# Kernel optimization log

Hardware: AMD Instinct MI355X
Metric: run time of the kernel (lower is better)

The kernel has to match this reference:

```python
import jax, jax.numpy as jnp
import numpy as np

B, T, C, H = 4, 4096, 1024, 128

def setup_inputs() -> dict:
    key = jax.random.key(0)
    k1, k2, k3, k4 = jax.random.split(key, 4)
    x = jax.random.normal(k1, (B, T, C), dtype=jnp.float32)
    # nn.Linear(embed, head, bias=False): y = x @ W, store W as [C, H]
    s = 1.0 / np.sqrt(C)
    Wk = jax.random.normal(k2, (C, H), dtype=jnp.float32) * s
    Wq = jax.random.normal(k3, (C, H), dtype=jnp.float32) * s
    Wv = jax.random.normal(k4, (C, H), dtype=jnp.float32) * s
    return {"x": x, "Wk": Wk, "Wq": Wq, "Wv": Wv}

def reference(x, Wk, Wq, Wv):
    Bx, Tx, Cx = x.shape
    scale = Wk.shape[1] ** -0.5
    k = x @ Wk  # [B,T,H]
    q = x @ Wq
    v = x @ Wv
    att = jnp.einsum('bth,bsh->bts', q, k) * scale  # [B,T,T]
    causal = jnp.triu(jnp.ones((Tx, Tx), dtype=bool), k=1)
    att = jnp.where(causal, -jnp.inf, att)
    att = jax.nn.softmax(att, axis=-1)
    # dropout is identity in eval mode
    out = jnp.einsum('bts,bsh->bth', att, v)  # [B,T,H]
    return out
```

## Files before the change

### kernel.cpp

```cpp
#include <hip/hip_runtime.h>
#include <stdint.h>
#include <math.h>

#define B_ 4
#define T_ 4096
#define C_ 1024
#define H_ 128

typedef __attribute__((ext_vector_type(8))) short s16x8;
typedef __attribute__((ext_vector_type(4))) float f32x4;

__device__ __forceinline__ unsigned short f2bf(float f) {
    union { float f; unsigned u; } v; v.f = f;
    unsigned r = v.u + 0x7fffu + ((v.u >> 16) & 1u);
    return (unsigned short)(r >> 16);
}

__device__ __forceinline__ s16x8 as_frag(uint4 u) {
    union { uint4 u; s16x8 s; } v; v.u = u; return v.s;
}

__host__ __device__ constexpr int chunks_total(int CH) {
    int a = 64 / CH, b = 64 % CH;
    return CH * a * (a + 1) / 2 + b * (a + 1);
}

#define QSC (0.0883883476f * 1.4426950408f)

__global__ __launch_bounds__(256) void k_wt(const float* __restrict__ Wk,
                                            const float* __restrict__ Wq,
                                            const float* __restrict__ Wv,
                                            unsigned short* __restrict__ Wt) {
    __shared__ float tile[64][65];
    int w = blockIdx.z;
    const float* W = (w == 0) ? Wk : (w == 1) ? Wq : Wv;
    int c0 = blockIdx.x * 64, h0 = blockIdx.y * 64;
    int tid = threadIdx.x;
#pragma unroll
    for (int k = 0; k < 16; k++) {
        int idx = tid + k * 256;
        int r = idx >> 6, c = idx & 63;
        tile[r][c] = W[(size_t)(c0 + r) * H_ + h0 + c];
    }
    __syncthreads();
#pragma unroll
    for (int k = 0; k < 16; k++) {
        int idx = tid + k * 256;
        int hh = idx >> 6, cc = idx & 63;
        Wt[(size_t)(w * H_ + h0 + hh) * C_ + c0 + cc] = f2bf(tile[cc][hh]);
    }
}

__global__ __launch_bounds__(512, 4) void k_qkv(const float* __restrict__ x,
                                                const unsigned short* __restrict__ Wt,
                                                unsigned short* __restrict__ Qb,
                                                unsigned short* __restrict__ Kb,
                                                unsigned short* __restrict__ Vt) {
    __shared__ unsigned short a_lds[2][32 * 72];
    int tid = threadIdx.x;
    int wv = tid >> 6, lane = tid & 63, quad = lane >> 4, lo = lane & 15;
    int r0 = blockIdx.x * 32;

    f32x4 acc[3][2];
#pragma unroll
    for (int i = 0; i < 3; i++)
#pragma unroll
        for (int j = 0; j < 2; j++) acc[i][j] = (f32x4){0.f, 0.f, 0.f, 0.f};

    const int row_s = tid >> 4;
    const int seg_s = (tid & 15) * 4;
    size_t xbase = (size_t)(r0 + row_s) * C_ + seg_s;

    const unsigned short* wp[3];
#pragma unroll
    for (int nt = 0; nt < 3; nt++)
        wp[nt] = Wt + (size_t)((wv * 3 + nt) * 16 + lo) * C_ + quad * 8;

    auto load_x = [&](int kc) -> float4 {
        return *(const float4*)(x + xbase + kc * 64);
    };
    auto pack_store = [&](unsigned short* buf, float4 f) {
        uint2 u;
        u.x = (unsigned)f2bf(f.x) | ((unsigned)f2bf(f.y) << 16);
        u.y = (unsigned)f2bf(f.z) | ((unsigned)f2bf(f.w) << 16);
        *(uint2*)&buf[row_s * 72 + seg_s] = u;
    };
    auto compute = [&](const unsigned short* buf, int kc) {
        s16x8 b[3][2];
#pragma unroll
        for (int nt = 0; nt < 3; nt++)
#pragma unroll
            for (int kh = 0; kh < 2; kh++)
                b[nt][kh] = *(const s16x8*)(wp[nt] + kc * 64 + kh * 32);
        s16x8 af[2][2];
#pragma unroll
        for (int mt = 0; mt < 2; mt++)
#pragma unroll
            for (int kh = 0; kh < 2; kh++)
                af[mt][kh] = *(const s16x8*)&buf[(mt * 16 + lo) * 72 + kh * 32 + quad * 8];
#pragma unroll
        for (int nt = 0; nt < 3; nt++)
#pragma unroll
            for (int kh = 0; kh < 2; kh++)
#pragma unroll
                for (int mt = 0; mt < 2; mt++)
                    acc[nt][mt] = __builtin_amdgcn_mfma_f32_16x16x32_bf16(
                        af[mt][kh], b[nt][kh], acc[nt][mt], 0, 0, 0);
    };

    float4 p0 = load_x(0);
    float4 p1 = load_x(1);
    pack_store(a_lds[0], p0);
    __syncthreads();

    for (int kc2 = 0; kc2 < 8; kc2++) {
        int kc = kc2 * 2;
        if (kc + 2 < 16) p0 = load_x(kc + 2);
        compute(a_lds[0], kc);
        pack_store(a_lds[1], p1);
        __syncthreads();
        if (kc + 3 < 16) p1 = load_x(kc + 3);
        compute(a_lds[1], kc + 1);
        if (kc + 2 < 16) pack_store(a_lds[0], p0);
        __syncthreads();
    }

#pragma unroll
    for (int nt = 0; nt < 3; nt++) {
        int col = (wv * 3 + nt) * 16 + lo;
        int w = col >> 7, h = col & 127;
#pragma unroll
        for (int mt = 0; mt < 2; mt++) {
            int mrow = r0 + mt * 16 + quad * 4;
            if (w == 2) {
                int b = mrow >> 12, t0 = mrow & 4095;
                int tp = (t0 & ~31) + (((t0 & 15) >> 2) << 3) + (((t0 >> 4) & 1) << 2);
                uint2 pk;
                pk.x = (unsigned)f2bf(acc[nt][mt][0]) | ((unsigned)f2bf(acc[nt][mt][1]) << 16);
                pk.y = (unsigned)f2bf(acc[nt][mt][2]) | ((unsigned)f2bf(acc[nt][mt][3]) << 16);
                *(uint2*)(Vt + (size_t)(b * H_ + h) * T_ + tp) = pk;
            } else if (w == 1) {
                unsigned short* dst = Qb + (size_t)mrow * H_ + h;
#pragma unroll
                for (int r = 0; r < 4; r++)
                    dst[(size_t)r * H_] = f2bf(acc[nt][mt][r] * QSC);
            } else {
                unsigned short* dst = Kb + (size_t)mrow * H_ + h;
#pragma unroll
                for (int r = 0; r < 4; r++)
                    dst[(size_t)r * H_] = f2bf(acc[nt][mt][r]);
            }
        }
    }
}

#define LOAD_KV(kv0)                                                            \
    do {                                                                        \
        const uint4* kg = (const uint4*)(Kb + (size_t)(batch * T_ + (kv0) + srow_k) * H_); \
        pk0 = kg[sseg_k + 0]; pk1 = kg[sseg_k + 1];                             \
        pk2 = kg[sseg_k + 2]; pk3 = kg[sseg_k + 3];                             \
        const uint4* vg = (const uint4*)(Vt + (size_t)(batch * H_ + srow_v) * T_ + (kv0)); \
        pv0 = vg[sseg_v + 0]; pv1 = vg[sseg_v + 1];                             \
        pv2 = vg[sseg_v + 2]; pv3 = vg[sseg_v + 3];                             \
    } while (0)

template <int CH>
__global__ __launch_bounds__(256, 3) void k_attn(const unsigned short* __restrict__ Qb,
                                                 const unsigned short* __restrict__ Kb,
                                                 const unsigned short* __restrict__ Vt,
                                                 float* __restrict__ Opart,
                                                 float* __restrict__ Mpart,
                                                 float* __restrict__ Lpart,
                                                 float* __restrict__ out) {
    __shared__ uint4 kbuf[64 * 16];
    __shared__ uint4 vbuf[128 * 8];

    int tid = threadIdx.x;
    int wv = tid >> 6, lane = tid & 63, quad = lane >> 4, lo = lane & 15;

    int id = blockIdx.x;
    int qt, batch, tbeg, tend, slot = 0;
    if constexpr (CH > 0) {
        slot = id >> 2; batch = id & 3;
        int s = slot, q = 63;
        for (;;) { int nc = (q + CH) / CH; if (s < nc) break; s -= nc; --q; }
        qt = q;
        tbeg = s * CH;
        tend = min(tbeg + CH, qt + 1);
    } else {
        qt = 63 - (id >> 2); batch = id & 3;
        tbeg = 0; tend = qt + 1;
    }
    int m0 = qt * 64 + wv * 16;
    int query = m0 + lo;

    s16x8 qf[4];
    size_t qrow = (size_t)(batch * T_ + m0 + lo) * H_;
#pragma unroll
    for (int ks = 0; ks < 4; ks++)
        qf[ks] = *(const s16x8*)(Qb + qrow + ks * 32 + quad * 8);

    f32x4 acc_o[8];
#pragma unroll
    for (int o = 0; o < 8; o++) acc_o[o] = (f32x4){0.f, 0.f, 0.f, 0.f};
    float m_i = -INFINITY, l_i = 0.f;

    const int srow_k = tid >> 2, sseg_k = (tid & 3) * 4;
    const int srow_v = tid >> 1, sseg_v = (tid & 1) * 4;

    uint4 pk0, pk1, pk2, pk3, pv0, pv1, pv2, pv3;
    LOAD_KV(tbeg * 64);

    for (int t = tbeg; t < tend; ++t) {
        int kv0 = t * 64;
        kbuf[srow_k * 16 + ((sseg_k + 0) ^ (srow_k & 15))] = pk0;
        kbuf[srow_k * 16 + ((sseg_k + 1) ^ (srow_k & 15))] = pk1;
        kbuf[srow_k * 16 + ((sseg_k + 2) ^ (srow_k & 15))] = pk2;
        kbuf[srow_k * 16 + ((sseg_k + 3) ^ (srow_k & 15))] = pk3;
        vbuf[srow_v * 8 + ((sseg_v + 0) ^ (srow_v & 7))] = pv0;
        vbuf[srow_v * 8 + ((sseg_v + 1) ^ (srow_v & 7))] = pv1;
        vbuf[srow_v * 8 + ((sseg_v + 2) ^ (srow_v & 7))] = pv2;
        vbuf[srow_v * 8 + ((sseg_v + 3) ^ (srow_v & 7))] = pv3;
        __syncthreads();
        if (t + 1 < tend) LOAD_KV((t + 1) * 64);

        f32x4 s_acc[4];
#pragma unroll
        for (int nt = 0; nt < 4; nt++) s_acc[nt] = (f32x4){0.f, 0.f, 0.f, 0.f};
#pragma unroll
        for (int ks = 0; ks < 4; ks++) {
#pragma unroll
            for (int nt = 0; nt < 4; nt++) {
                s16x8 kf = as_frag(kbuf[(nt * 16 + lo) * 16 + ((ks * 4 + quad) ^ lo)]);
                s_acc[nt] = __builtin_amdgcn_mfma_f32_16x16x32_bf16(kf, qf[ks], s_acc[nt], 0, 0, 0);
            }
        }

        float p[4][4];
        bool diag = (t == qt);
#pragma unroll
        for (int nt = 0; nt < 4; nt++)
#pragma unroll
            for (int r = 0; r < 4; r++) {
                float sv = s_acc[nt][r];
                if (diag && (kv0 + nt * 16 + quad * 4 + r > query)) sv = -INFINITY;
                p[nt][r] = sv;
            }

        float mx = p[0][0];
#pragma unroll
        for (int nt = 0; nt < 4; nt++)
#pragma unroll
            for (int r = 0; r < 4; r++) mx = fmaxf(mx, p[nt][r]);
        if (__any(mx > m_i + 8.0f)) {
            float rm = fmaxf(mx, __shfl_xor(mx, 16));
            rm = fmaxf(rm, __shfl_xor(rm, 32));
            float mnew = fmaxf(m_i, rm);
            float alpha = exp2f(m_i - mnew);
            l_i *= alpha;
            m_i = mnew;
#pragma unroll
            for (int o = 0; o < 8; o++)
#pragma unroll
                for (int r = 0; r < 4; r++) acc_o[o][r] *= alpha;
        }
        float rs = 0.f;
#pragma unroll
        for (int nt = 0; nt < 4; nt++)
#pragma unroll
            for (int r = 0; r < 4; r++) {
                float pv = exp2f(p[nt][r] - m_i);
                p[nt][r] = pv;
                rs += pv;
            }
        l_i += rs;

        s16x8 pf[2];
#pragma unroll
        for (int kt = 0; kt < 2; kt++) {
            uint4 u;
            u.x = (__float_as_uint(p[2 * kt][0]) >> 16) | ((__float_as_uint(p[2 * kt][1]) >> 16) << 16);
            u.y = (__float_as_uint(p[2 * kt][2]) >> 16) | ((__float_as_uint(p[2 * kt][3]) >> 16) << 16);
            u.z = (__float_as_uint(p[2 * kt + 1][0]) >> 16) | ((__float_as_uint(p[2 * kt + 1][1]) >> 16) << 16);
            u.w = (__float_as_uint(p[2 * kt + 1][2]) >> 16) | ((__float_as_uint(p[2 * kt + 1][3]) >> 16) << 16);
            pf[kt] = as_frag(u);
        }

#pragma unroll
        for (int kt = 0; kt < 2; kt++)
#pragma unroll
            for (int o = 0; o < 8; o++) {
                int vrow = o * 16 + lo;
                s16x8 vf = as_frag(vbuf[vrow * 8 + ((kt * 4 + quad) ^ (vrow & 7))]);
                acc_o[o] = __builtin_amdgcn_mfma_f32_16x16x32_bf16(vf, pf[kt], acc_o[o], 0, 0, 0);
            }
        __syncthreads();
    }

    l_i += __shfl_xor(l_i, 16);
    l_i += __shfl_xor(l_i, 32);

    if constexpr (CH > 0) {
        constexpr int NCH = chunks_total(CH);
        size_t pr = (size_t)(batch * NCH + slot) * 64 + wv * 16 + lo;
        float* Op = Opart + pr * 128;
#pragma unroll
        for (int o = 0; o < 8; o++) {
            float4 v = {acc_o[o][0], acc_o[o][1], acc_o[o][2], acc_o[o][3]};
            *(float4*)(Op + o * 16 + quad * 4) = v;
        }
        if (quad == 0) { Mpart[pr] = m_i; Lpart[pr] = l_i; }
    } else {
        float inv = 1.0f / l_i;
        int rowg = batch * T_ + m0 + lo;
#pragma unroll
        for (int o = 0; o < 8; o++) {
            float4 v = {acc_o[o][0] * inv, acc_o[o][1] * inv,
                        acc_o[o][2] * inv, acc_o[o][3] * inv};
            *(float4*)(out + (size_t)rowg * H_ + o * 16 + quad * 4) = v;
        }
    }
}

template <int CH>
__global__ __launch_bounds__(256) void k_comb(const float* __restrict__ Opart,
                                              const float* __restrict__ Mpart,
                                              const float* __restrict__ Lpart,
                                              float* __restrict__ out) {
    constexpr int NCH = chunks_total(CH);
    int tid = threadIdx.x;
    int row = blockIdx.x * 8 + (tid >> 5);
    int h4 = (tid & 31) * 4;
    int batch = row >> 12, t = row & 4095, qt = t >> 6;
    int n = qt + 1;
    int nc = (qt + CH) / CH;
    int a = n / CH, b = n % CH;
    int S = CH * a * (a + 1) / 2 + b * (a + 1);
    int base = NCH - S;
    float M = -INFINITY, den = 0.f;
    float4 o = {0.f, 0.f, 0.f, 0.f};
    for (int s = 0; s < nc; ++s) {
        size_t pr = (size_t)(batch * NCH + base + s) * 64 + (t & 63);
        float ms = Mpart[pr], ls = Lpart[pr];
        float4 v = *(const float4*)(Opart + pr * 128 + h4);
        float Mn = fmaxf(M, ms);
        float wa = exp2f(M - Mn), wb = exp2f(ms - Mn);
        den = den * wa + ls * wb;
        o.x = o.x * wa + v.x * wb;
        o.y = o.y * wa + v.y * wb;
        o.z = o.z * wa + v.z * wb;
        o.w = o.w * wa + v.w * wb;
        M = Mn;
    }
    float inv = 1.0f / den;
    float4 r = {o.x * inv, o.y * inv, o.z * inv, o.w * inv};
    *(float4*)(out + (size_t)row * H_ + h4) = r;
}

extern "C" void kernel_launch(void* const* d_in, const int* in_sizes, int n_in,
                              void* d_out, int out_size, void* d_ws, size_t ws_size,
                              hipStream_t stream) {
    const float* x  = (const float*)d_in[0];
    const float* Wk = (const float*)d_in[1];
    const float* Wq = (const float*)d_in[2];
    const float* Wv = (const float*)d_in[3];
    char* ws = (char*)d_ws;
    unsigned short* Wt = (unsigned short*)ws;
    unsigned short* Qb = (unsigned short*)(ws + (1u << 20));
    unsigned short* Kb = (unsigned short*)(ws + (5u << 20));
    unsigned short* Vt = (unsigned short*)(ws + (9u << 20));
    float* out = (float*)d_out;

    const size_t base = (size_t)13 << 20;
    constexpr int NCH10 = chunks_total(10);
    constexpr int NCH21 = chunks_total(21);
    auto need_for = [&](int nch) {
        return base + (size_t)4 * nch * 64 * (128 * 4) + 2 * (size_t)4 * nch * 64 * 4;
    };

    k_wt  <<<dim3(16, 2, 3), 256, 0, stream>>>(Wk, Wq, Wv, Wt);
    k_qkv <<<dim3(512), 512, 0, stream>>>(x, Wt, Qb, Kb, Vt);

    if (ws_size >= need_for(NCH10)) {
        float* Op = (float*)(ws + base);
        float* Mp = Op + (size_t)4 * NCH10 * 64 * 128;
        float* Lp = Mp + (size_t)4 * NCH10 * 64;
        k_attn<10><<<4 * NCH10, 256, 0, stream>>>(Qb, Kb, Vt, Op, Mp, Lp, out);
        k_comb<10><<<2048, 256, 0, stream>>>(Op, Mp, Lp, out);
    } else if (ws_size >= need_for(NCH21)) {
        float* Op = (float*)(ws + base);
        float* Mp = Op + (size_t)4 * NCH21 * 64 * 128;
        float* Lp = Mp + (size_t)4 * NCH21 * 64;
        k_attn<21><<<4 * NCH21, 256, 0, stream>>>(Qb, Kb, Vt, Op, Mp, Lp, out);
        k_comb<21><<<2048, 256, 0, stream>>>(Op, Mp, Lp, out);
    } else {
        k_attn<0><<<256, 256, 0, stream>>>(Qb, Kb, Vt, nullptr, nullptr, nullptr, out);
    }
}
```

Measured before the change: 190.6 us.

## Retile QKV projection into 64-row blocks split across columns, add MFMA priority hints

The QKV projection kernel now uses 256-thread blocks that each cover 64 rows and one half of the 384 output columns, launched as a 256x2 grid. Each thread loads 16 floats per step, and every weight fragment feeds four M tiles instead of two, so weights are reused more. The attention kernel raises its occupancy hint to 4 and wraps its MFMA loops in s_setprio so those waves get issue priority. The causal mask is also hoisted into a separate diagonal-only branch. In exchange, x is read twice (once per column half), and more accumulator registers are used per thread.

```diff
diff --git a/kernel.cpp b/kernel.cpp
--- a/kernel.cpp
+++ b/kernel.cpp
@@ -51,39 +51,50 @@
     }
 }
 
-__global__ __launch_bounds__(512, 4) void k_qkv(const float* __restrict__ x,
+__global__ __launch_bounds__(256, 3) void k_qkv(const float* __restrict__ x,
                                                 const unsigned short* __restrict__ Wt,
                                                 unsigned short* __restrict__ Qb,
                                                 unsigned short* __restrict__ Kb,
                                                 unsigned short* __restrict__ Vt) {
-    __shared__ unsigned short a_lds[2][32 * 72];
+    __shared__ unsigned short a_lds[2][64 * 72];
     int tid = threadIdx.x;
     int wv = tid >> 6, lane = tid & 63, quad = lane >> 4, lo = lane & 15;
-    int r0 = blockIdx.x * 32;
-
-    f32x4 acc[3][2];
+    int r0 = blockIdx.x * 64;
+    int cb = blockIdx.y;
+    int nt0 = wv * 3;
+
+    f32x4 acc[3][4];
 #pragma unroll
     for (int i = 0; i < 3; i++)
 #pragma unroll
-        for (int j = 0; j < 2; j++) acc[i][j] = (f32x4){0.f, 0.f, 0.f, 0.f};
-
-    const int row_s = tid >> 4;
-    const int seg_s = (tid & 15) * 4;
+        for (int j = 0; j < 4; j++) acc[i][j] = (f32x4){0.f, 0.f, 0.f, 0.f};
+
+    const int row_s = tid >> 2;
+    const int seg_s = (tid & 3) * 16;
     size_t xbase = (size_t)(r0 + row_s) * C_ + seg_s;
 
     const unsigned short* wp[3];
 #pragma unroll
     for (int nt = 0; nt < 3; nt++)
-        wp[nt] = Wt + (size_t)((wv * 3 + nt) * 16 + lo) * C_ + quad * 8;
-
-    auto load_x = [&](int kc) -> float4 {
-        return *(const float4*)(x + xbase + kc * 64);
+        wp[nt] = Wt + (size_t)(cb * 192 + (nt0 + nt) * 16 + lo) * C_ + quad * 8;
+
+    auto pack_store = [&](unsigned short* buf, const float4 (&f)[4]) {
+        uint4 u0, u1;
+        u0.x = (unsigned)f2bf(f[0].x) | ((unsigned)f2bf(f[0].y) << 16);
+        u0.y = (unsigned)f2bf(f[0].z) | ((unsigned)f2bf(f[0].w) << 16);
+        u0.z = (unsigned)f2bf(f[1].x) | ((unsigned)f2bf(f[1].y) << 16);
+        u0.w = (unsigned)f2bf(f[1].z) | ((unsigned)f2bf(f[1].w) << 16);
+        u1.x = (unsigned)f2bf(f[2].x) | ((unsigned)f2bf(f[2].y) << 16);
+        u1.y = (unsigned)f2bf(f[2].z) | ((unsigned)f2bf(f[2].w) << 16);
+        u1.z = (unsigned)f2bf(f[3].x) | ((unsigned)f2bf(f[3].y) << 16);
+        u1.w = (unsigned)f2bf(f[3].z) | ((unsigned)f2bf(f[3].w) << 16);
+        *(uint4*)&buf[row_s * 72 + seg_s] = u0;
+        *(uint4*)&buf[row_s * 72 + seg_s + 8] = u1;
     };
-    auto pack_store = [&](unsigned short* buf, float4 f) {
-        uint2 u;
-        u.x = (unsigned)f2bf(f.x) | ((unsigned)f2bf(f.y) << 16);
-        u.y = (unsigned)f2bf(f.z) | ((unsigned)f2bf(f.w) << 16);
-        *(uint2*)&buf[row_s * 72 + seg_s] = u;
+    auto load_x = [&](float4 (&f)[4], int kc) {
+        const float* xp = x + xbase + kc * 64;
+#pragma unroll
+        for (int j = 0; j < 4; j++) f[j] = *(const float4*)(xp + j * 4);
     };
     auto compute = [&](const unsigned short* buf, int kc) {
         s16x8 b[3][2];
@@ -92,9 +103,9 @@
 #pragma unroll
             for (int kh = 0; kh < 2; kh++)
                 b[nt][kh] = *(const s16x8*)(wp[nt] + kc * 64 + kh * 32);
-        s16x8 af[2][2];
-#pragma unroll
-        for (int mt = 0; mt < 2; mt++)
+        s16x8 af[4][2];
+#pragma unroll
+        for (int mt = 0; mt < 4; mt++)
 #pragma unroll
             for (int kh = 0; kh < 2; kh++)
                 af[mt][kh] = *(const s16x8*)&buf[(mt * 16 + lo) * 72 + kh * 32 + quad * 8];
@@ -103,34 +114,35 @@
 #pragma unroll
             for (int kh = 0; kh < 2; kh++)
 #pragma unroll
-                for (int mt = 0; mt < 2; mt++)
+                for (int mt = 0; mt < 4; mt++)
                     acc[nt][mt] = __builtin_amdgcn_mfma_f32_16x16x32_bf16(
                         af[mt][kh], b[nt][kh], acc[nt][mt], 0, 0, 0);
     };
 
-    float4 p0 = load_x(0);
-    float4 p1 = load_x(1);
-    pack_store(a_lds[0], p0);
+    float4 x0[4], x1[4];
+    load_x(x0, 0);
+    load_x(x1, 1);
+    pack_store(a_lds[0], x0);
     __syncthreads();
 
     for (int kc2 = 0; kc2 < 8; kc2++) {
         int kc = kc2 * 2;
-        if (kc + 2 < 16) p0 = load_x(kc + 2);
+        if (kc + 2 < 16) load_x(x0, kc + 2);
         compute(a_lds[0], kc);
-        pack_store(a_lds[1], p1);
+        pack_store(a_lds[1], x1);
         __syncthreads();
-        if (kc + 3 < 16) p1 = load_x(kc + 3);
+        if (kc + 3 < 16) load_x(x1, kc + 3);
         compute(a_lds[1], kc + 1);
-        if (kc + 2 < 16) pack_store(a_lds[0], p0);
+        if (kc + 2 < 16) pack_store(a_lds[0], x0);
         __syncthreads();
     }
 
 #pragma unroll
     for (int nt = 0; nt < 3; nt++) {
-        int col = (wv * 3 + nt) * 16 + lo;
+        int col = cb * 192 + (nt0 + nt) * 16 + lo;
         int w = col >> 7, h = col & 127;
 #pragma unroll
-        for (int mt = 0; mt < 2; mt++) {
+        for (int mt = 0; mt < 4; mt++) {
             int mrow = r0 + mt * 16 + quad * 4;
             if (w == 2) {
                 int b = mrow >> 12, t0 = mrow & 4095;
@@ -165,7 +177,7 @@
     } while (0)
 
 template <int CH>
-__global__ __launch_bounds__(256, 3) void k_attn(const unsigned short* __restrict__ Qb,
+__global__ __launch_bounds__(256, 4) void k_attn(const unsigned short* __restrict__ Qb,
                                                  const unsigned short* __restrict__ Kb,
                                                  const unsigned short* __restrict__ Vt,
                                                  float* __restrict__ Opart,
@@ -227,6 +239,7 @@
         f32x4 s_acc[4];
 #pragma unroll
         for (int nt = 0; nt < 4; nt++) s_acc[nt] = (f32x4){0.f, 0.f, 0.f, 0.f};
+        __builtin_amdgcn_s_setprio(1);
 #pragma unroll
         for (int ks = 0; ks < 4; ks++) {
 #pragma unroll
@@ -235,17 +248,20 @@
                 s_acc[nt] = __builtin_amdgcn_mfma_f32_16x16x32_bf16(kf, qf[ks], s_acc[nt], 0, 0, 0);
             }
         }
+        __builtin_amdgcn_s_setprio(0);
 
         float p[4][4];
-        bool diag = (t == qt);
 #pragma unroll
         for (int nt = 0; nt < 4; nt++)
 #pragma unroll
-            for (int r = 0; r < 4; r++) {
-                float sv = s_acc[nt][r];
-                if (diag && (kv0 + nt * 16 + quad * 4 + r > query)) sv = -INFINITY;
-                p[nt][r] = sv;
-            }
+            for (int r = 0; r < 4; r++) p[nt][r] = s_acc[nt][r];
+        if (t == qt) {
+#pragma unroll
+            for (int nt = 0; nt < 4; nt++)
+#pragma unroll
+                for (int r = 0; r < 4; r++)
+                    if (kv0 + nt * 16 + quad * 4 + r > query) p[nt][r] = -INFINITY;
+        }
 
         float mx = p[0][0];
 #pragma unroll
@@ -286,6 +302,7 @@
             pf[kt] = as_frag(u);
         }
 
+        __builtin_amdgcn_s_setprio(1);
 #pragma unroll
         for (int kt = 0; kt < 2; kt++)
 #pragma unroll
@@ -294,6 +311,7 @@
                 s16x8 vf = as_frag(vbuf[vrow * 8 + ((kt * 4 + quad) ^ (vrow & 7))]);
                 acc_o[o] = __builtin_amdgcn_mfma_f32_16x16x32_bf16(vf, pf[kt], acc_o[o], 0, 0, 0);
             }
+        __builtin_amdgcn_s_setprio(0);
         __syncthreads();
     }
 
@@ -379,7 +397,7 @@
     };
 
     k_wt  <<<dim3(16, 2, 3), 256, 0, stream>>>(Wk, Wq, Wv, Wt);
-    k_qkv <<<dim3(512), 512, 0, stream>>>(x, Wt, Qb, Kb, Vt);
+    k_qkv <<<dim3(256, 2), 256, 0, stream>>>(x, Wt, Qb, Kb, Vt);
 
     if (ws_size >= need_for(NCH10)) {
         float* Op = (float*)(ws + base);
```

After: 174.6 us. -8.4%, faster.
